# Performance work log

Measured on AMD Instinct MI355X. Metric: run time of the kernel, lower is better.

## Reference

```python
import jax, jax.numpy as jnp
import numpy as np

EMBED_DIM = 1024
NUM_HEADS = 16
D_K = EMBED_DIM // NUM_HEADS
SCALE = D_K ** -0.5
WEIGHT_EPS = 1e-5


def setup_inputs() -> dict:
    key = jax.random.key(0)
    ks = jax.random.split(key, 12)
    B, T, E = 4, 1024, EMBED_DIM
    init = 1.0 / np.sqrt(E)  # ~ nn.Linear default scale
    inp = {
        "q": jax.random.normal(ks[0], (B, T, E), jnp.float32),
        "k": jax.random.normal(ks[1], (B, T, E), jnp.float32),
        "v": jax.random.normal(ks[2], (B, T, E), jnp.float32),
        "weights": jax.random.uniform(ks[3], (B, T), jnp.float32),
        "Wq": jax.random.uniform(ks[4], (E, E), jnp.float32, -init, init),
        "bq": jax.random.uniform(ks[5], (E,), jnp.float32, -init, init),
        "Wk": jax.random.uniform(ks[6], (E, E), jnp.float32, -init, init),
        "bk": jax.random.uniform(ks[7], (E,), jnp.float32, -init, init),
        "Wv": jax.random.uniform(ks[8], (E, E), jnp.float32, -init, init),
        "bv": jax.random.uniform(ks[9], (E,), jnp.float32, -init, init),
        "Wo": jax.random.uniform(ks[10], (E, E), jnp.float32, -init, init),
        "bo": jax.random.uniform(ks[11], (E,), jnp.float32, -init, init),
    }
    return inp


def reference(q, k, v, weights, Wq, bq, Wk, bk, Wv, bv, Wo, bo):
    B, T, E = q.shape
    H, Dk = NUM_HEADS, D_K
    # linear projections (torch Linear: x @ W.T + b), split into heads
    qh = (q @ Wq.T + bq).reshape(B, T, H, Dk).transpose(0, 2, 1, 3)  # [B,H,T,Dk]
    kh = (k @ Wk.T + bk).reshape(B, T, H, Dk).transpose(0, 2, 1, 3)
    vh = (v @ Wv.T + bv).reshape(B, T, H, Dk).transpose(0, 2, 1, 3)
    # scaled energy [B,H,Tq,Tk]
    energy = jnp.einsum("bhqd,bhkd->bhqk", qh, kh) * SCALE
    # weight^2 gating over key axis + masked_fill(-inf) where weight < eps
    w = weights[:, None, None, :]  # [B,1,1,Tk]
    energy = jnp.where(w < WEIGHT_EPS, -jnp.inf, energy * (w * w))
    attn = jax.nn.softmax(energy, axis=-1)  # dropout is identity in eval mode
    out = jnp.einsum("bhqk,bhkd->bhqd", attn, vh)  # [B,H,T,Dk]
    out = out.transpose(0, 2, 1, 3).reshape(B, T, E)
    return out @ Wo.T + bo
```

## Files before the change

kernel.cpp:

```cpp
#include <hip/hip_runtime.h>
#include <hip/hip_bf16.h>
#include <stdint.h>

using frag = __attribute__((ext_vector_type(8))) short;
using f4   = __attribute__((ext_vector_type(4))) float;
using bf16 = __hip_bfloat16;

static constexpr float WEPS = 1e-5f;
static constexpr float SC2K  = 0.125f * 1.44269504f;
static constexpr float EBIAS = -8.0f * 1.44269504f;

#define AS1(p) ((const __attribute__((address_space(1))) void*)(p))
#define AS3(p) ((__attribute__((address_space(3))) void*)(p))

__device__ __forceinline__ void gl2lds16(const void* g, void* l) {
    __builtin_amdgcn_global_load_lds(AS1(g), AS3(l), 16, 0, 0);
}

__device__ inline uint4 pack8(float4 a, float4 b) {
    union { bf16 h[8]; uint4 u; } x;
    x.h[0] = __float2bfloat16(a.x); x.h[1] = __float2bfloat16(a.y);
    x.h[2] = __float2bfloat16(a.z); x.h[3] = __float2bfloat16(a.w);
    x.h[4] = __float2bfloat16(b.x); x.h[5] = __float2bfloat16(b.y);
    x.h[6] = __float2bfloat16(b.z); x.h[7] = __float2bfloat16(b.w);
    return x.u;
}

__device__ __forceinline__ uint2 pack4(float a, float b, float c, float d) {
    union { bf16 h[4]; uint2 u; } x;
    x.h[0] = __float2bfloat16(a); x.h[1] = __float2bfloat16(b);
    x.h[2] = __float2bfloat16(c); x.h[3] = __float2bfloat16(d);
    return x.u;
}

__device__ __forceinline__ int tperm(int t) {
    return (t & ~63) | (((t & 15) << 2) | ((t >> 4) & 3));
}

struct CvtArgs {
    const float* src[7];
    long long    bounds[8];
    long long    total;
};

__global__ __launch_bounds__(256) void cvt_kernel(CvtArgs a, bf16* __restrict__ dst)
{
    long long e = ((long long)blockIdx.x * 256 + threadIdx.x) * 8;
    if (e >= a.total) return;
    int s = 0;
    while (e >= a.bounds[s + 1]) s++;
    const float* src = a.src[s] + (e - a.bounds[s]);
    float4 f0 = ((const float4*)src)[0];
    float4 f1 = ((const float4*)src)[1];
    *(uint4*)(dst + e) = pack8(f0, f1);
}

struct GemmBatch {
    const void*  A[3];
    const void*  W[3];
    const float* bias[3];
    void*        Out[3];
    int          mode[3];
};

template<bool ABF, bool WBF>
__global__ __launch_bounds__(256) void gemm_batch(GemmBatch g)
{
    constexpr int K = 1024;
    __shared__ bf16 As[2][128 * 32];
    __shared__ bf16 Bs[2][128 * 32];

    const int z = blockIdx.z;
    const void*  Ap   = g.A[z];
    const void*  Wp   = g.W[z];
    const float* bias = g.bias[z];
    void*        OutP = g.Out[z];
    const int    mode = g.mode[z];

    const int tid = threadIdx.x;
    const int lid = blockIdx.x + 8 * blockIdx.y;
    const int big   = (lid & 7) * 4 + (lid >> 6);
    const int small = (lid >> 3) & 7;
    int m0, n0;
    if (mode == 4) { m0 = small * 128; n0 = big * 128; }
    else           { m0 = big * 128;   n0 = small * 128; }

    const int lane = tid & 63;
    const int wave = tid >> 6;
    const int wm   = (wave >> 1) * 64;
    const int wn   = (wave & 1) * 64;
    const int lr   = lane & 15;
    const int q    = lane >> 4;

    const int sr = tid >> 1;
    const int sc = (tid & 1) * 16;

    const int c0 = wave * 128 + lane;
    const int c1 = c0 + 64;
    const int r0 = c0 >> 2, col0 = (c0 & 3) * 8;
    const int r1 = c1 >> 2, col1 = (c1 & 3) * 8;

    auto stage = [&](int k0, int pb) {
        if (WBF) {
            const bf16* W = (const bf16*)Wp;
            gl2lds16(&W[(size_t)(n0 + r0) * K + k0 + col0], &Bs[pb][wave * 1024]);
            gl2lds16(&W[(size_t)(n0 + r1) * K + k0 + col1], &Bs[pb][wave * 1024 + 512]);
        } else {
            const float* W = (const float*)Wp;
            const float* src = &W[(size_t)(n0 + sr) * K + k0 + sc];
            float4 f0 = ((const float4*)src)[0];
            float4 f1 = ((const float4*)src)[1];
            float4 f2 = ((const float4*)src)[2];
            float4 f3 = ((const float4*)src)[3];
            *(uint4*)(&Bs[pb][sr * 32 + sc])     = pack8(f0, f1);
            *(uint4*)(&Bs[pb][sr * 32 + sc + 8]) = pack8(f2, f3);
        }
        if (ABF) {
            const bf16* A = (const bf16*)Ap;
            gl2lds16(&A[(size_t)(m0 + r0) * K + k0 + col0], &As[pb][wave * 1024]);
            gl2lds16(&A[(size_t)(m0 + r1) * K + k0 + col1], &As[pb][wave * 1024 + 512]);
        } else {
            const float* A = (const float*)Ap;
            const float* src = &A[(size_t)(m0 + sr) * K + k0 + sc];
            float4 f0 = ((const float4*)src)[0];
            float4 f1 = ((const float4*)src)[1];
            float4 f2 = ((const float4*)src)[2];
            float4 f3 = ((const float4*)src)[3];
            *(uint4*)(&As[pb][sr * 32 + sc])     = pack8(f0, f1);
            *(uint4*)(&As[pb][sr * 32 + sc + 8]) = pack8(f2, f3);
        }
    };

    f4 acc[4][4];
    #pragma unroll
    for (int i = 0; i < 4; i++)
        #pragma unroll
        for (int j = 0; j < 4; j++) acc[i][j] = f4{0.f, 0.f, 0.f, 0.f};

    stage(0, 0);
    __syncthreads();

    for (int kt = 0; kt < 32; kt++) {
        const int cb = kt & 1;
        if (kt < 31) stage((kt + 1) * 32, cb ^ 1);

        frag af[4], bfr[4];
        #pragma unroll
        for (int i = 0; i < 4; i++)
            af[i] = *(const frag*)(&As[cb][(wm + i * 16 + lr) * 32 + q * 8]);
        #pragma unroll
        for (int j = 0; j < 4; j++)
            bfr[j] = *(const frag*)(&Bs[cb][(wn + j * 16 + lr) * 32 + q * 8]);
        #pragma unroll
        for (int i = 0; i < 4; i++)
            #pragma unroll
            for (int j = 0; j < 4; j++)
                acc[i][j] = __builtin_amdgcn_mfma_f32_16x16x32_bf16(af[i], bfr[j], acc[i][j], 0, 0, 0);
        __syncthreads();
    }

    if (mode == 4) {
        const int bbt   = (n0 + wn) >> 10;
        const int tbase = (n0 + wn) & 1023;
        bf16* O = (bf16*)OutP;
        #pragma unroll
        for (int i = 0; i < 4; i++) {
            int row0 = m0 + wm + i * 16 + q * 4;
            #pragma unroll
            for (int r = 0; r < 4; r++) {
                int f = row0 + r;
                int h = f >> 6, d = f & 63;
                float bv = bias[f];
                size_t idx = ((((size_t)bbt * 16 + h) * 64 + d) << 10) + tbase + lr * 4;
                *(uint2*)(&O[idx]) = pack4(acc[i][0][r] + bv, acc[i][1][r] + bv,
                                           acc[i][2][r] + bv, acc[i][3][r] + bv);
            }
        }
    } else {
        #pragma unroll
        for (int i = 0; i < 4; i++) {
            int row0 = m0 + wm + i * 16 + q * 4;
            #pragma unroll
            for (int j = 0; j < 4; j++) {
                int col = n0 + wn + j * 16 + lr;
                float bv = bias[col];
                #pragma unroll
                for (int r = 0; r < 4; r++) {
                    float val = acc[i][j][r] + bv;
                    int mrow = row0 + r;
                    if (mode == 3) {
                        ((float*)OutP)[(size_t)mrow * 1024 + col] = val;
                    } else {
                        int bb = mrow >> 10, t = mrow & 1023;
                        int h  = col >> 6,   d = col & 63;
                        size_t idx;
                        if (mode == 2)
                            idx = ((((size_t)bb * 16 + h) * 64 + d) << 10) + tperm(t);
                        else
                            idx = ((((size_t)bb * 16 + h) << 10) + t) * 64 + d;
                        ((bf16*)OutP)[idx] = __float2bfloat16(val);
                    }
                }
            }
        }
    }
}

template<bool WBF>
__global__ __launch_bounds__(256) void gemm_out(const bf16* __restrict__ A,
                                                const void* __restrict__ Wp,
                                                const float* __restrict__ bias,
                                                float* __restrict__ Out)
{
    constexpr int K = 1024;
    __shared__ bf16 As0[64 * 64], As1[64 * 64], As2[64 * 64];
    __shared__ bf16 Bs0[128 * 64], Bs1[128 * 64], Bs2[128 * 64];

    const int tid = threadIdx.x;
    const int lid = blockIdx.x + 8 * blockIdx.y;
    const int mt  = (lid & 7) * 8 + (lid >> 6);
    const int nt  = (lid >> 3) & 7;
    const int n0  = nt * 128;
    const int m0  = mt * 64;
    const int lane = tid & 63;
    const int wave = tid >> 6;
    const int wm   = (wave >> 1) * 32;
    const int wn   = (wave & 1) * 64;
    const int lr   = lane & 15;
    const int q    = lane >> 4;

    const int sr = tid >> 1;
    const int sc = (tid & 1) * 32;

    int rb[4], cb4[4];
    #pragma unroll
    for (int gg = 0; gg < 4; gg++) {
        int D = wave * 256 + gg * 64 + lane;
        rb[gg]  = D >> 3;
        cb4[gg] = (D & 7) * 8;
    }
    int ra[2], ca4[2];
    #pragma unroll
    for (int gg = 0; gg < 2; gg++) {
        int D = wave * 128 + gg * 64 + lane;
        ra[gg]  = D >> 3;
        ca4[gg] = (D & 7) * 8;
    }

    auto stage = [&](int k0, bf16* Asd, bf16* Bsd) {
        if (WBF) {
            const bf16* W = (const bf16*)Wp;
            #pragma unroll
            for (int gg = 0; gg < 4; gg++)
                gl2lds16(&W[(size_t)(n0 + rb[gg]) * K + k0 + cb4[gg]],
                         &Bsd[(wave * 256 + gg * 64) * 8]);
        } else {
            const float* W = (const float*)Wp;
            const float* src = &W[(size_t)(n0 + sr) * K + k0 + sc];
            #pragma unroll
            for (int c = 0; c < 4; c++) {
                float4 f0 = ((const float4*)src)[2 * c];
                float4 f1 = ((const float4*)src)[2 * c + 1];
                *(uint4*)(&Bsd[sr * 64 + sc + c * 8]) = pack8(f0, f1);
            }
        }
        #pragma unroll
        for (int gg = 0; gg < 2; gg++)
            gl2lds16(&A[(size_t)(m0 + ra[gg]) * K + k0 + ca4[gg]],
                     &Asd[(wave * 128 + gg * 64) * 8]);
    };

    f4 acc[2][4];
    #pragma unroll
    for (int i = 0; i < 2; i++)
        #pragma unroll
        for (int j = 0; j < 4; j++) acc[i][j] = f4{0.f, 0.f, 0.f, 0.f};

    auto compute = [&](const bf16* Asp, const bf16* Bsp) {
        #pragma unroll
        for (int kk = 0; kk < 2; kk++) {
            frag af[2], bfr[4];
            #pragma unroll
            for (int i = 0; i < 2; i++)
                af[i] = *(const frag*)(&Asp[(wm + i * 16 + lr) * 64 + kk * 32 + q * 8]);
            #pragma unroll
            for (int j = 0; j < 4; j++)
                bfr[j] = *(const frag*)(&Bsp[(wn + j * 16 + lr) * 64 + kk * 32 + q * 8]);
            #pragma unroll
            for (int i = 0; i < 2; i++)
                #pragma unroll
                for (int j = 0; j < 4; j++)
                    acc[i][j] = __builtin_amdgcn_mfma_f32_16x16x32_bf16(af[i], bfr[j], acc[i][j], 0, 0, 0);
        }
    };

    if (WBF) {
        stage(0,   As0, Bs0);
        stage(64,  As1, Bs1);
        asm volatile("s_waitcnt vmcnt(6)" ::: "memory");
        __builtin_amdgcn_s_barrier();

        for (int m = 0; m < 4; m++) {
            const int kb = m * 192;
            stage(kb + 128, As2, Bs2);
            compute(As0, Bs0);
            asm volatile("s_waitcnt vmcnt(6)" ::: "memory");
            __builtin_amdgcn_s_barrier();

            stage(kb + 192, As0, Bs0);
            compute(As1, Bs1);
            asm volatile("s_waitcnt vmcnt(6)" ::: "memory");
            __builtin_amdgcn_s_barrier();

            stage(kb + 256, As1, Bs1);
            compute(As2, Bs2);
            asm volatile("s_waitcnt vmcnt(6)" ::: "memory");
            __builtin_amdgcn_s_barrier();
        }
        stage(896, As2, Bs2);
        compute(As0, Bs0);
        asm volatile("s_waitcnt vmcnt(6)" ::: "memory");
        __builtin_amdgcn_s_barrier();
        stage(960, As0, Bs0);
        compute(As1, Bs1);
        asm volatile("s_waitcnt vmcnt(6)" ::: "memory");
        __builtin_amdgcn_s_barrier();
        compute(As2, Bs2);
        asm volatile("s_waitcnt vmcnt(0)" ::: "memory");
        __builtin_amdgcn_s_barrier();
        compute(As0, Bs0);
    } else {
        stage(0,   As0, Bs0);
        stage(64,  As1, Bs1);
        __syncthreads();
        for (int m = 0; m < 4; m++) {
            const int kb = m * 192;
            stage(kb + 128, As2, Bs2);
            compute(As0, Bs0);
            __syncthreads();
            stage(kb + 192, As0, Bs0);
            compute(As1, Bs1);
            __syncthreads();
            stage(kb + 256, As1, Bs1);
            compute(As2, Bs2);
            __syncthreads();
        }
        stage(896, As2, Bs2);
        compute(As0, Bs0);
        __syncthreads();
        stage(960, As0, Bs0);
        compute(As1, Bs1);
        __syncthreads();
        compute(As2, Bs2);
        __syncthreads();
        compute(As0, Bs0);
    }

    #pragma unroll
    for (int i = 0; i < 2; i++) {
        int row0 = m0 + wm + i * 16 + q * 4;
        #pragma unroll
        for (int j = 0; j < 4; j++) {
            int col = n0 + wn + j * 16 + lr;
            float bv = bias[col];
            #pragma unroll
            for (int r = 0; r < 4; r++)
                Out[(size_t)(row0 + r) * 1024 + col] = acc[i][j][r] + bv;
        }
    }
}

__global__ __launch_bounds__(256, 3) void attn_kernel(const bf16* __restrict__ qh,
                                                      const bf16* __restrict__ kh,
                                                      const bf16* __restrict__ vhT,
                                                      const float* __restrict__ wts,
                                                      bf16* __restrict__ att)
{
    constexpr int LDP = 72;
    __shared__ bf16 Ks[2][64 * 64];
    __shared__ bf16 Vs[2][64 * 64];
    __shared__ bf16 Plds[4][32 * LDP];

    const int tid  = threadIdx.x;
    const int lane = tid & 63;
    const int wave = tid >> 6;
    const int lr   = lane & 15;
    const int q    = lane >> 4;
    const int bh   = blockIdx.x;
    const int bb   = bh >> 4;
    const int h    = bh & 15;
    const int q0w  = blockIdx.y * 128 + wave * 32;
    const size_t base = (size_t)bh * 1024 * 64;

    const int cA = wave * 128 + lane;
    const int cB = cA + 64;
    const int rowA = cA >> 3, gA = ((cA & 7) ^ (rowA & 7)) * 8;
    const int rowB = cB >> 3, gB = ((cB & 7) ^ (rowB & 7)) * 8;

    frag aq[2][2];
    #pragma unroll
    for (int rf = 0; rf < 2; rf++)
        #pragma unroll
        for (int ks = 0; ks < 2; ks++)
            aq[rf][ks] = *(const frag*)(&qh[base + (size_t)(q0w + rf * 16 + lr) * 64 + ks * 32 + q * 8]);

    float rs[2][4];
    f4 o[2][4];
    #pragma unroll
    for (int rf = 0; rf < 2; rf++)
        #pragma unroll
        for (int j = 0; j < 4; j++) {
            o[rf][j] = f4{0.f, 0.f, 0.f, 0.f};
            rs[rf][j] = 0.f;
        }

    gl2lds16(&kh [base + (size_t)rowA * 64 + gA],   &Ks[0][wave * 1024]);
    gl2lds16(&kh [base + (size_t)rowB * 64 + gB],   &Ks[0][wave * 1024 + 512]);
    gl2lds16(&vhT[base + (size_t)rowA * 1024 + gA], &Vs[0][wave * 1024]);
    gl2lds16(&vhT[base + (size_t)rowB * 1024 + gB], &Vs[0][wave * 1024 + 512]);
    __syncthreads();

    for (int t = 0; t < 16; t++) {
        const int k0  = t * 64;
        const int buf = t & 1;
        if (t < 15) {
            int kn = k0 + 64;
            gl2lds16(&kh [base + (size_t)(kn + rowA) * 64 + gA],  &Ks[buf ^ 1][wave * 1024]);
            gl2lds16(&kh [base + (size_t)(kn + rowB) * 64 + gB],  &Ks[buf ^ 1][wave * 1024 + 512]);
            gl2lds16(&vhT[base + (size_t)rowA * 1024 + kn + gA], &Vs[buf ^ 1][wave * 1024]);
            gl2lds16(&vhT[base + (size_t)rowB * 1024 + kn + gB], &Vs[buf ^ 1][wave * 1024 + 512]);
        }

        float sc2[4], eb[4];
        #pragma unroll
        for (int j = 0; j < 4; j++) {
            float w = wts[bb * 1024 + k0 + j * 16 + lr];
            sc2[j] = SC2K * w * w;
            eb[j]  = (w < WEPS) ? -1e30f : EBIAS;
        }

        frag kb[4][2];
        #pragma unroll
        for (int j = 0; j < 4; j++) {
            int rowj = j * 16 + lr;
            kb[j][0] = *(const frag*)(&Ks[buf][rowj * 64 + (((q    ) ^ (rowj & 7)) * 8)]);
            kb[j][1] = *(const frag*)(&Ks[buf][rowj * 64 + (((q + 4) ^ (rowj & 7)) * 8)]);
        }

        #pragma unroll
        for (int rf = 0; rf < 2; rf++) {
            f4 s[4];
            __builtin_amdgcn_s_setprio(1);
            #pragma unroll
            for (int j = 0; j < 4; j++) {
                f4 z = f4{0.f, 0.f, 0.f, 0.f};
                s[j] = __builtin_amdgcn_mfma_f32_16x16x32_bf16(aq[rf][0], kb[j][0], z, 0, 0, 0);
                s[j] = __builtin_amdgcn_mfma_f32_16x16x32_bf16(aq[rf][1], kb[j][1], s[j], 0, 0, 0);
            }
            __builtin_amdgcn_s_setprio(0);
            float p[4][4];
            #pragma unroll
            for (int j = 0; j < 4; j++)
                #pragma unroll
                for (int r = 0; r < 4; r++) {
                    p[j][r] = __builtin_amdgcn_exp2f(fmaf(s[j][r], sc2[j], eb[j]));
                    rs[rf][r] += p[j][r];
                }
            #pragma unroll
            for (int r = 0; r < 4; r++)
                *(uint2*)(&Plds[wave][(rf * 16 + q * 4 + r) * LDP + lr * 4]) =
                    pack4(p[0][r], p[1][r], p[2][r], p[3][r]);
        }

        frag vb[4][2];
        #pragma unroll
        for (int j = 0; j < 4; j++) {
            int rowj = j * 16 + lr;
            vb[j][0] = *(const frag*)(&Vs[buf][rowj * 64 + (((q    ) ^ (rowj & 7)) * 8)]);
            vb[j][1] = *(const frag*)(&Vs[buf][rowj * 64 + (((q + 4) ^ (rowj & 7)) * 8)]);
        }

        #pragma unroll
        for (int rf = 0; rf < 2; rf++) {
            frag ap0 = *(const frag*)(&Plds[wave][(rf * 16 + lr) * LDP + q * 8]);
            frag ap1 = *(const frag*)(&Plds[wave][(rf * 16 + lr) * LDP + 32 + q * 8]);
            __builtin_amdgcn_s_setprio(1);
            #pragma unroll
            for (int j = 0; j < 4; j++) {
                o[rf][j] = __builtin_amdgcn_mfma_f32_16x16x32_bf16(ap0, vb[j][0], o[rf][j], 0, 0, 0);
                o[rf][j] = __builtin_amdgcn_mfma_f32_16x16x32_bf16(ap1, vb[j][1], o[rf][j], 0, 0, 0);
            }
            __builtin_amdgcn_s_setprio(0);
        }
        __syncthreads();
    }

    #pragma unroll
    for (int off = 1; off < 16; off <<= 1)
        #pragma unroll
        for (int rf = 0; rf < 2; rf++)
            #pragma unroll
            for (int r = 0; r < 4; r++)
                rs[rf][r] += __shfl_xor(rs[rf][r], off, 64);

    #pragma unroll
    for (int rf = 0; rf < 2; rf++) {
        float inv[4];
        #pragma unroll
        for (int r = 0; r < 4; r++) inv[r] = 1.0f / rs[rf][r];
        const int t0 = q0w + rf * 16 + q * 4;
        #pragma unroll
        for (int j = 0; j < 4; j++) {
            int d = h * 64 + j * 16 + lr;
            #pragma unroll
            for (int r = 0; r < 4; r++)
                att[((size_t)bb * 1024 + t0 + r) * 1024 + d] =
                    __float2bfloat16(o[rf][j][r] * inv[r]);
        }
    }
}

extern "C" void kernel_launch(void* const* d_in, const int* in_sizes, int n_in,
                              void* d_out, int out_size, void* d_ws, size_t ws_size,
                              hipStream_t stream)
{
    const float* q   = (const float*)d_in[0];
    const float* k   = (const float*)d_in[1];
    const float* v   = (const float*)d_in[2];
    const float* wts = (const float*)d_in[3];
    const float* Wq  = (const float*)d_in[4];
    const float* bq  = (const float*)d_in[5];
    const float* Wk  = (const float*)d_in[6];
    const float* bk  = (const float*)d_in[7];
    const float* Wv  = (const float*)d_in[8];
    const float* bv  = (const float*)d_in[9];
    const float* Wo  = (const float*)d_in[10];
    const float* bo  = (const float*)d_in[11];
    float* out = (float*)d_out;

    const long long Mi = 1024 * 1024;
    bf16* qh  = (bf16*)d_ws;
    bf16* kh  = qh  + 4 * Mi;
    bf16* vhT = kh  + 4 * Mi;
    bf16* att = vhT + 4 * Mi;
    bf16* cvt = att + 4 * Mi;
    const size_t base_bytes = (size_t)32 * Mi;

    dim3 blk(256);

    if (ws_size >= base_bytes + (size_t)32 * Mi) {
        CvtArgs ca{};
        ca.src[0] = q;  ca.src[1] = k;  ca.src[2] = v;
        ca.src[3] = Wq; ca.src[4] = Wk; ca.src[5] = Wv; ca.src[6] = Wo;
        long long bnd[8] = {0, 4*Mi, 8*Mi, 12*Mi, 13*Mi, 14*Mi, 15*Mi, 16*Mi};
        for (int i = 0; i < 8; i++) ca.bounds[i] = bnd[i];
        ca.total = 16 * Mi;
        cvt_kernel<<<8192, blk, 0, stream>>>(ca, cvt);

        GemmBatch gq{};
        gq.A[0] = cvt;          gq.A[1] = cvt + 4*Mi;   gq.A[2] = cvt + 14*Mi;
        gq.W[0] = cvt + 12*Mi;  gq.W[1] = cvt + 13*Mi;  gq.W[2] = cvt + 8*Mi;
        gq.bias[0] = bq; gq.bias[1] = bk; gq.bias[2] = bv;
        gq.Out[0] = qh;  gq.Out[1] = kh;  gq.Out[2] = vhT;
        gq.mode[0] = 0;  gq.mode[1] = 0;  gq.mode[2] = 4;
        gemm_batch<true, true><<<dim3(8, 32, 3), blk, 0, stream>>>(gq);

        attn_kernel<<<dim3(64, 8), blk, 0, stream>>>(qh, kh, vhT, wts, att);

        gemm_out<true><<<dim3(8, 64), blk, 0, stream>>>(att, cvt + 15*Mi, bo, out);
    } else if (ws_size >= base_bytes + (size_t)8 * Mi) {
        CvtArgs ca{};
        ca.src[0] = Wq; ca.src[1] = Wk; ca.src[2] = Wv; ca.src[3] = Wo;
        long long bnd[8] = {0, 1*Mi, 2*Mi, 3*Mi, 4*Mi, 4*Mi, 4*Mi, 4*Mi};
        for (int i = 0; i < 8; i++) ca.bounds[i] = bnd[i];
        ca.total = 4 * Mi;
        cvt_kernel<<<2048, blk, 0, stream>>>(ca, cvt);

        GemmBatch gq{};
        gq.A[0] = q; gq.A[1] = k; gq.A[2] = v;
        gq.W[0] = cvt; gq.W[1] = cvt + 1*Mi; gq.W[2] = cvt + 2*Mi;
        gq.bias[0] = bq; gq.bias[1] = bk; gq.bias[2] = bv;
        gq.Out[0] = qh;  gq.Out[1] = kh;  gq.Out[2] = vhT;
        gq.mode[0] = 0;  gq.mode[1] = 0;  gq.mode[2] = 2;
        gemm_batch<false, true><<<dim3(8, 32, 3), blk, 0, stream>>>(gq);

        attn_kernel<<<dim3(64, 8), blk, 0, stream>>>(qh, kh, vhT, wts, att);

        gemm_out<true><<<dim3(8, 64), blk, 0, stream>>>(att, cvt + 3*Mi, bo, out);
    } else {
        GemmBatch gq{};
        gq.A[0] = q; gq.A[1] = k; gq.A[2] = v;
        gq.W[0] = Wq; gq.W[1] = Wk; gq.W[2] = Wv;
        gq.bias[0] = bq; gq.bias[1] = bk; gq.bias[2] = bv;
        gq.Out[0] = qh;  gq.Out[1] = kh;  gq.Out[2] = vhT;
        gq.mode[0] = 0;  gq.mode[1] = 0;  gq.mode[2] = 2;
        gemm_batch<false, false><<<dim3(8, 32, 3), blk, 0, stream>>>(gq);

        attn_kernel<<<dim3(64, 8), blk, 0, stream>>>(qh, kh, vhT, wts, att);

        gemm_out<false><<<dim3(8, 64), blk, 0, stream>>>(att, Wo, bo, out);
    }
}
```

Baseline: 207.2 us.

## Drop full-activation bf16 pre-conversion; convert only weights and read fp32 activations

Removes the workspace path that converted q, k, v and all weights to bf16 in a separate pass. Only the weights are converted now, and the QKV GEMM reads fp32 activations directly; the V projection uses the transposed mode 4 with bf16 Wv as the A operand. The A/W precision flags become runtime per-batch values instead of template parameters. This saves a large conversion pass over the activations, at the cost of runtime branching and fp32 loads inside the GEMM.

New measurement: 221.8 us. +7.1%, slower.

```diff
diff --git a/kernel.cpp b/kernel.cpp
--- a/kernel.cpp
+++ b/kernel.cpp
@@ -61,9 +61,10 @@
     const float* bias[3];
     void*        Out[3];
     int          mode[3];
+    int          abf[3];
+    int          wbf[3];
 };
 
-template<bool ABF, bool WBF>
 __global__ __launch_bounds__(256) void gemm_batch(GemmBatch g)
 {
     constexpr int K = 1024;
@@ -76,6 +77,8 @@
     const float* bias = g.bias[z];
     void*        OutP = g.Out[z];
     const int    mode = g.mode[z];
+    const bool   ABF  = g.abf[z] != 0;
+    const bool   WBF  = g.wbf[z] != 0;
 
     const int tid = threadIdx.x;
     const int lid = blockIdx.x + 8 * blockIdx.y;
@@ -548,27 +551,7 @@
 
     dim3 blk(256);
 
-    if (ws_size >= base_bytes + (size_t)32 * Mi) {
-        CvtArgs ca{};
-        ca.src[0] = q;  ca.src[1] = k;  ca.src[2] = v;
-        ca.src[3] = Wq; ca.src[4] = Wk; ca.src[5] = Wv; ca.src[6] = Wo;
-        long long bnd[8] = {0, 4*Mi, 8*Mi, 12*Mi, 13*Mi, 14*Mi, 15*Mi, 16*Mi};
-        for (int i = 0; i < 8; i++) ca.bounds[i] = bnd[i];
-        ca.total = 16 * Mi;
-        cvt_kernel<<<8192, blk, 0, stream>>>(ca, cvt);
-
-        GemmBatch gq{};
-        gq.A[0] = cvt;          gq.A[1] = cvt + 4*Mi;   gq.A[2] = cvt + 14*Mi;
-        gq.W[0] = cvt + 12*Mi;  gq.W[1] = cvt + 13*Mi;  gq.W[2] = cvt + 8*Mi;
-        gq.bias[0] = bq; gq.bias[1] = bk; gq.bias[2] = bv;
-        gq.Out[0] = qh;  gq.Out[1] = kh;  gq.Out[2] = vhT;
-        gq.mode[0] = 0;  gq.mode[1] = 0;  gq.mode[2] = 4;
-        gemm_batch<true, true><<<dim3(8, 32, 3), blk, 0, stream>>>(gq);
-
-        attn_kernel<<<dim3(64, 8), blk, 0, stream>>>(qh, kh, vhT, wts, att);
-
-        gemm_out<true><<<dim3(8, 64), blk, 0, stream>>>(att, cvt + 15*Mi, bo, out);
-    } else if (ws_size >= base_bytes + (size_t)8 * Mi) {
+    if (ws_size >= base_bytes + (size_t)8 * Mi) {
         CvtArgs ca{};
         ca.src[0] = Wq; ca.src[1] = Wk; ca.src[2] = Wv; ca.src[3] = Wo;
         long long bnd[8] = {0, 1*Mi, 2*Mi, 3*Mi, 4*Mi, 4*Mi, 4*Mi, 4*Mi};
@@ -577,12 +560,14 @@
         cvt_kernel<<<2048, blk, 0, stream>>>(ca, cvt);
 
         GemmBatch gq{};
-        gq.A[0] = q; gq.A[1] = k; gq.A[2] = v;
-        gq.W[0] = cvt; gq.W[1] = cvt + 1*Mi; gq.W[2] = cvt + 2*Mi;
+        gq.A[0] = q;            gq.A[1] = k;            gq.A[2] = cvt + 2*Mi;
+        gq.W[0] = cvt;          gq.W[1] = cvt + 1*Mi;   gq.W[2] = v;
         gq.bias[0] = bq; gq.bias[1] = bk; gq.bias[2] = bv;
         gq.Out[0] = qh;  gq.Out[1] = kh;  gq.Out[2] = vhT;
-        gq.mode[0] = 0;  gq.mode[1] = 0;  gq.mode[2] = 2;
-        gemm_batch<false, true><<<dim3(8, 32, 3), blk, 0, stream>>>(gq);
+        gq.mode[0] = 0;  gq.mode[1] = 0;  gq.mode[2] = 4;
+        gq.abf[0] = 0;   gq.abf[1] = 0;   gq.abf[2] = 1;
+        gq.wbf[0] = 1;   gq.wbf[1] = 1;   gq.wbf[2] = 0;
+        gemm_batch<<<dim3(8, 32, 3), blk, 0, stream>>>(gq);
 
         attn_kernel<<<dim3(64, 8), blk, 0, stream>>>(qh, kh, vhT, wts, att);
 
@@ -594,7 +579,9 @@
         gq.bias[0] = bq; gq.bias[1] = bk; gq.bias[2] = bv;
         gq.Out[0] = qh;  gq.Out[1] = kh;  gq.Out[2] = vhT;
         gq.mode[0] = 0;  gq.mode[1] = 0;  gq.mode[2] = 2;
-        gemm_batch<false, false><<<dim3(8, 32, 3), blk, 0, stream>>>(gq);
+        gq.abf[0] = 0;   gq.abf[1] = 0;   gq.abf[2] = 0;
+        gq.wbf[0] = 0;   gq.wbf[1] = 0;   gq.wbf[2] = 0;
+        gemm_batch<<<dim3(8, 32, 3), blk, 0, stream>>>(gq);
 
         attn_kernel<<<dim3(64, 8), blk, 0, stream>>>(qh, kh, vhT, wts, att);
 
```
